# Kernel optimization log

Hardware: AMD Instinct MI355X
Metric: run time of the kernel (lower is better)

## Reference

```python
import jax, jax.numpy as jnp
import numpy as np

EMBED_DIM = 64  # scale factor dim (matches head dim)


def setup_inputs() -> dict:
    key0 = jax.random.key(0)
    kq, kk, kv = jax.random.split(key0, 3)
    shape = (2, 16, 2048, 64)  # [B, H, S, D]
    return {
        "query": jax.random.normal(kq, shape, dtype=jnp.float32),
        "key": jax.random.normal(kk, shape, dtype=jnp.float32),
        "value": jax.random.normal(kv, shape, dtype=jnp.float32),
    }


def reference(query, key, value):
    # qk = Q K^T / sqrt(embed_dim); softmax over last dim; @ V
    inv_scale = jnp.sqrt(jnp.asarray(EMBED_DIM, dtype=query.dtype))
    scores = jnp.einsum("bhqd,bhkd->bhqk", query, key) / inv_scale
    probs = jax.nn.softmax(scores, axis=-1)
    # dropout_p=0.0 -> identity (eval semantics)
    return jnp.einsum("bhqk,bhkd->bhqd", probs, value)
```

## Files before the change

kernel.cpp:

```cpp
#include <hip/hip_runtime.h>
#include <hip/hip_bf16.h>

#define S_LEN 2048
#define DDIM  64
#define NT    (S_LEN / 64)
#define SCALE  0.125f
#define SCALE2 0.18033688f
#define NELEM  4194304
#define NQROW  65536
#define WC_LGKM0 0xc07f

#if __has_builtin(__builtin_amdgcn_permlane32_swap) && __has_builtin(__builtin_amdgcn_permlane16_swap)
#define HAVE_PLSWAP 1
#else
#define HAVE_PLSWAP 0
#endif

typedef __attribute__((ext_vector_type(8))) short short8;
typedef __attribute__((ext_vector_type(4))) float floatx4;

__device__ __forceinline__ short f2bf(float f) {
    union { float f; unsigned u; } v; v.f = f;
    return (short)((v.u + 0x7fffu + ((v.u >> 16) & 1u)) >> 16);
}

__device__ __forceinline__ unsigned pk2bf(float a, float b) {
    union { float f; unsigned u; } x, y; x.f = a; y.f = b;
    unsigned lo = (x.u + 0x7fffu + ((x.u >> 16) & 1u)) >> 16;
    unsigned hi = (y.u + 0x7fffu + ((y.u >> 16) & 1u)) & 0xffff0000u;
    return lo | hi;
}

__device__ __forceinline__ float fexp2(float x) {
#if __has_builtin(__builtin_amdgcn_exp2f)
    return __builtin_amdgcn_exp2f(x);
#else
    return exp2f(x);
#endif
}

#if HAVE_PLSWAP
__device__ __forceinline__ void plswap32(unsigned &a, unsigned &b) {
    auto r = __builtin_amdgcn_permlane32_swap((int)a, (int)b, false, false);
    a = (unsigned)r[0]; b = (unsigned)r[1];
}
__device__ __forceinline__ void plswap16(unsigned &a, unsigned &b) {
    auto r = __builtin_amdgcn_permlane16_swap((int)a, (int)b, false, false);
    a = (unsigned)r[0]; b = (unsigned)r[1];
}
#endif

__global__ __launch_bounds__(256) void prep_kv(const float* __restrict__ K,
                                               const float* __restrict__ V,
                                               short* __restrict__ Kb,
                                               short* __restrict__ Vt) {
    const int bh = blockIdx.x & 31;
    const int st = blockIdx.x >> 5;
    const int t  = threadIdx.x;
    const size_t tile_off = (size_t)bh * (S_LEN * DDIM) + (size_t)st * (64 * DDIM);

    {
        const float* src = K + tile_off + t * 16;
        short* dst = Kb + tile_off + t * 16;
        #pragma unroll
        for (int h = 0; h < 2; ++h) {
            float4 a = *(const float4*)(src + h * 8);
            float4 b = *(const float4*)(src + h * 8 + 4);
            uint4 o;
            o.x = pk2bf(a.x, a.y); o.y = pk2bf(a.z, a.w);
            o.z = pk2bf(b.x, b.y); o.w = pk2bf(b.z, b.w);
            *(uint4*)(dst + h * 8) = o;
        }
    }

    {
        const int s4 = (t & 15) * 4;
        const int d4 = (t >> 4) * 4;
        const float* src = V + tile_off;
        float4 v0 = *(const float4*)(src + (size_t)(s4 + 0) * 64 + d4);
        float4 v1 = *(const float4*)(src + (size_t)(s4 + 1) * 64 + d4);
        float4 v2 = *(const float4*)(src + (size_t)(s4 + 2) * 64 + d4);
        float4 v3 = *(const float4*)(src + (size_t)(s4 + 3) * 64 + d4);
        const float* r0 = (const float*)&v0;
        const float* r1 = (const float*)&v1;
        const float* r2 = (const float*)&v2;
        const float* r3 = (const float*)&v3;
        short* dstb = Vt + (size_t)bh * (DDIM * S_LEN) + (size_t)st * 64 + s4;
        #pragma unroll
        for (int dd = 0; dd < 4; ++dd) {
            uint2 o;
            o.x = pk2bf(r0[dd], r1[dd]);
            o.y = pk2bf(r2[dd], r3[dd]);
            *(uint2*)(dstb + (size_t)(d4 + dd) * S_LEN) = o;
        }
    }
}

__global__ __launch_bounds__(512) void attn_sm8(
    const float* __restrict__ Q, const short* __restrict__ Kb,
    const short* __restrict__ Vt, float* __restrict__ O)
{
    __shared__ short Ks[2][64 * 64];
    __shared__ short Vs[2][64 * 64];
    __shared__ float Dl[128];
#if !HAVE_PLSWAP
    __shared__ short Pl[8][32 * 64];
#endif

    constexpr int NIT = NT / 2;

    const int tid  = threadIdx.x;
    const int wave = tid >> 6;
    const int grp  = wave >> 2;
    const int w4   = wave & 3;
    const int lane = tid & 63;
    const int l16  = lane & 15;
    const int quad = lane >> 4;
    const int x7   = l16 & 7;

    const int bh = blockIdx.x & 31;
    const int qt = blockIdx.x >> 5;
    const int ks = grp;
    const size_t base = (size_t)bh * (S_LEN * DDIM);

    const int g   = tid & 255;
    const int ci0 = g,        r0 = ci0 >> 3, c0 = (ci0 & 7) ^ (r0 & 7);
    const int ci1 = 256 + g,  r1 = ci1 >> 3, c1 = (ci1 & 7) ^ (r1 & 7);
    const size_t koff = (size_t)ks * NIT * (64 * 64);
    const size_t voff = (size_t)ks * NIT * 64;
    const short* pK0 = Kb + base + koff + r0 * 64 + c0 * 8;
    const short* pK1 = Kb + base + koff + r1 * 64 + c1 * 8;
    const short* pV0 = Vt + base + voff + (size_t)r0 * S_LEN + c0 * 8;
    const short* pV1 = Vt + base + voff + (size_t)r1 * S_LEN + c1 * 8;

    short8 rk0 = *(const short8*)pK0;
    short8 rk1 = *(const short8*)pK1;
    short8 rv0 = *(const short8*)pV0;
    short8 rv1 = *(const short8*)pV1;

    short8 qf[2][2];
    #pragma unroll
    for (int nq = 0; nq < 2; ++nq) {
        const float* qp = Q + base + (size_t)(qt * 128 + w4 * 32 + nq * 16 + l16) * 64 + quad * 8;
        #pragma unroll
        for (int kt = 0; kt < 2; ++kt) {
            float4 a = *(const float4*)(qp + kt * 32);
            float4 b = *(const float4*)(qp + kt * 32 + 4);
            union { unsigned u[4]; short8 s; } qc;
            qc.u[0] = pk2bf(a.x * SCALE2, a.y * SCALE2);
            qc.u[1] = pk2bf(a.z * SCALE2, a.w * SCALE2);
            qc.u[2] = pk2bf(b.x * SCALE2, b.y * SCALE2);
            qc.u[3] = pk2bf(b.z * SCALE2, b.w * SCALE2);
            qf[nq][kt] = qc.s;
        }
    }

    floatx4 oacc[2][4];
    float rs[2];
    #pragma unroll
    for (int mt = 0; mt < 2; ++mt) {
        #pragma unroll
        for (int dt = 0; dt < 4; ++dt) oacc[mt][dt] = (floatx4){0.f,0.f,0.f,0.f};
        rs[mt] = 0.f;
    }

    short* Ksg = &Ks[grp][0];
    short* Vsg = &Vs[grp][0];
#if !HAVE_PLSWAP
    short* Pw = &Pl[wave][0];
#endif

    for (int kb = 0; kb < NIT; ++kb) {
        if (kb) __builtin_amdgcn_s_barrier();

        *(short8*)&Ksg[ci0 * 8] = rk0;
        *(short8*)&Ksg[ci1 * 8] = rk1;
        *(short8*)&Vsg[ci0 * 8] = rv0;
        *(short8*)&Vsg[ci1 * 8] = rv1;

        if (kb + 1 < NIT) {
            const int ok = (kb + 1) * (64 * 64), ov = (kb + 1) * 64;
            rk0 = *(const short8*)(pK0 + ok);
            rk1 = *(const short8*)(pK1 + ok);
            rv0 = *(const short8*)(pV0 + ov);
            rv1 = *(const short8*)(pV1 + ov);
        }

        __builtin_amdgcn_s_waitcnt(WC_LGKM0);
        __builtin_amdgcn_s_barrier();

        floatx4 sc[2][4];
        #pragma unroll
        for (int mk = 0; mk < 4; ++mk) {
            floatx4 a0 = (floatx4){0.f,0.f,0.f,0.f};
            floatx4 a1 = (floatx4){0.f,0.f,0.f,0.f};
            #pragma unroll
            for (int kt = 0; kt < 2; ++kt) {
                const int csw = (kt * 4 + quad) ^ x7;
                short8 kf = *(const short8*)&Ksg[(mk * 16 + l16) * 64 + csw * 8];
                a0 = __builtin_amdgcn_mfma_f32_16x16x32_bf16(kf, qf[0][kt], a0, 0, 0, 0);
                a1 = __builtin_amdgcn_mfma_f32_16x16x32_bf16(kf, qf[1][kt], a1, 0, 0, 0);
            }
            sc[0][mk] = a0; sc[1][mk] = a1;
        }

#if HAVE_PLSWAP
        unsigned pa[2][4], pb[2][4];
        #pragma unroll
        for (int nq = 0; nq < 2; ++nq) {
            #pragma unroll
            for (int mk = 0; mk < 4; ++mk) {
                float p0 = fexp2(sc[nq][mk][0]);
                float p1 = fexp2(sc[nq][mk][1]);
                float p2 = fexp2(sc[nq][mk][2]);
                float p3 = fexp2(sc[nq][mk][3]);
                rs[nq] += (p0 + p1) + (p2 + p3);
                pa[nq][mk] = pk2bf(p0, p1);
                pb[nq][mk] = pk2bf(p2, p3);
            }
        }

        #pragma unroll
        for (int kt = 0; kt < 2; ++kt) {
            short8 pf[2];
            #pragma unroll
            for (int nq = 0; nq < 2; ++nq) {
                unsigned a0 = pa[nq][2 * kt], a1 = pa[nq][2 * kt + 1];
                unsigned b0 = pb[nq][2 * kt], b1 = pb[nq][2 * kt + 1];
                plswap32(a0, a1); plswap16(a0, a1);
                plswap32(b0, b1); plswap16(b0, b1);
                union { unsigned u[4]; short8 s; } c;
                c.u[0] = a0; c.u[1] = b0; c.u[2] = a1; c.u[3] = b1;
                pf[nq] = c.s;
            }
            const int csw = (kt * 4 + quad) ^ x7;
            #pragma unroll
            for (int dt = 0; dt < 4; ++dt) {
                short8 vf = *(const short8*)&Vsg[(dt * 16 + l16) * 64 + csw * 8];
                oacc[0][dt] = __builtin_amdgcn_mfma_f32_16x16x32_bf16(pf[0], vf, oacc[0][dt], 0, 0, 0);
                oacc[1][dt] = __builtin_amdgcn_mfma_f32_16x16x32_bf16(pf[1], vf, oacc[1][dt], 0, 0, 0);
            }
        }
#else
        #pragma unroll
        for (int nq = 0; nq < 2; ++nq) {
            const int prow = (nq * 16 + l16) * 64;
            #pragma unroll
            for (int mk = 0; mk < 4; ++mk) {
                float p0 = fexp2(sc[nq][mk][0]);
                float p1 = fexp2(sc[nq][mk][1]);
                float p2 = fexp2(sc[nq][mk][2]);
                float p3 = fexp2(sc[nq][mk][3]);
                rs[nq] += (p0 + p1) + (p2 + p3);
                uint2 pv; pv.x = pk2bf(p0, p1); pv.y = pk2bf(p2, p3);
                const int c8 = (mk * 4 + quad) ^ (2 * x7);
                *(uint2*)&Pw[prow + c8 * 4] = pv;
            }
        }
        #pragma unroll
        for (int kt = 0; kt < 2; ++kt) {
            const int csw = (kt * 4 + quad) ^ x7;
            short8 pf0 = *(const short8*)&Pw[(l16)      * 64 + csw * 8];
            short8 pf1 = *(const short8*)&Pw[(16 + l16) * 64 + csw * 8];
            #pragma unroll
            for (int dt = 0; dt < 4; ++dt) {
                short8 vf = *(const short8*)&Vsg[(dt * 16 + l16) * 64 + csw * 8];
                oacc[0][dt] = __builtin_amdgcn_mfma_f32_16x16x32_bf16(pf0, vf, oacc[0][dt], 0, 0, 0);
                oacc[1][dt] = __builtin_amdgcn_mfma_f32_16x16x32_bf16(pf1, vf, oacc[1][dt], 0, 0, 0);
            }
        }
#endif
    }

    float sred[2];
    #pragma unroll
    for (int nq = 0; nq < 2; ++nq) {
        float s = rs[nq];
        s += __shfl_xor(s, 16, 64);
        s += __shfl_xor(s, 32, 64);
        sred[nq] = s;
    }

    if (grp == 1 && quad == 0) {
        Dl[w4 * 32 + l16]      = sred[0];
        Dl[w4 * 32 + 16 + l16] = sred[1];
    }
    __syncthreads();

    float invt[2];
    if (grp == 0) {
        invt[0] = 1.0f / (sred[0] + Dl[w4 * 32 + l16]);
        invt[1] = 1.0f / (sred[1] + Dl[w4 * 32 + 16 + l16]);
    }

    float* Nb = (float*)&Ks[0][0];
    #pragma unroll
    for (int mt = 0; mt < 2; ++mt) {
        if (grp == 1) {
            #pragma unroll
            for (int dt = 0; dt < 4; ++dt)
                #pragma unroll
                for (int r = 0; r < 4; ++r)
                    Nb[(dt * 4 + r) * 256 + w4 * 64 + lane] = oacc[mt][dt][r];
        }
        __syncthreads();
        if (grp == 0) {
            #pragma unroll
            for (int r = 0; r < 4; ++r) {
                const int row = qt * 128 + w4 * 32 + mt * 16 + quad * 4 + r;
                const float it = __shfl(invt[mt], quad * 4 + r, 64);
                float* op = O + base + (size_t)row * 64 + l16;
                #pragma unroll
                for (int dt = 0; dt < 4; ++dt)
                    op[dt * 16] = (oacc[mt][dt][r] + Nb[(dt * 4 + r) * 256 + w4 * 64 + lane]) * it;
            }
        }
        __syncthreads();
    }
}

#define BQ    64
#define BKEY  64
#define KPAD  72

__global__ __launch_bounds__(256) void attn_kernel(
    const float* __restrict__ Q, const float* __restrict__ K,
    const float* __restrict__ V, float* __restrict__ O)
{
    __shared__ short Ksh[BKEY * KPAD];
    __shared__ short Vtt[DDIM * KPAD];
    __shared__ short Pls[4][16 * KPAD];

    const int tid  = threadIdx.x;
    const int wave = tid >> 6;
    const int lane = tid & 63;
    const int l16  = lane & 15;
    const int quad = lane >> 4;

    const int bh = blockIdx.x & 31;
    const int qt = blockIdx.x >> 5;
    const size_t base = (size_t)bh * S_LEN * DDIM;

    const int qrow = qt * BQ + wave * 16 + l16;
    short8 qf[2];
    {
        const float* qp = Q + base + (size_t)qrow * DDIM + quad * 8;
        #pragma unroll
        for (int kt = 0; kt < 2; ++kt) {
            float4 a = *(const float4*)(qp + kt * 32);
            float4 b = *(const float4*)(qp + kt * 32 + 4);
            short* d = (short*)&qf[kt];
            d[0]=f2bf(a.x*SCALE); d[1]=f2bf(a.y*SCALE); d[2]=f2bf(a.z*SCALE); d[3]=f2bf(a.w*SCALE);
            d[4]=f2bf(b.x*SCALE); d[5]=f2bf(b.y*SCALE); d[6]=f2bf(b.z*SCALE); d[7]=f2bf(b.w*SCALE);
        }
    }

    float m_i[4], l_i[4];
    floatx4 oacc[4];
    #pragma unroll
    for (int r = 0; r < 4; ++r) { m_i[r] = -3.0e38f; l_i[r] = 0.f; }
    #pragma unroll
    for (int dt = 0; dt < 4; ++dt) oacc[dt] = (floatx4){0.f, 0.f, 0.f, 0.f};

    const int skey = tid >> 2;
    const int scol = (tid & 3) * 4;

    for (int kb = 0; kb < S_LEN / BKEY; ++kb) {
        const float* Kg = K + base + (size_t)kb * BKEY * DDIM + (size_t)skey * DDIM;
        const float* Vg = V + base + (size_t)kb * BKEY * DDIM + (size_t)skey * DDIM;
        #pragma unroll
        for (int i = 0; i < 4; ++i) {
            const int c = scol + i * 16;
            float4 kv = *(const float4*)(Kg + c);
            short* kd = &Ksh[skey * KPAD + c];
            kd[0]=f2bf(kv.x); kd[1]=f2bf(kv.y); kd[2]=f2bf(kv.z); kd[3]=f2bf(kv.w);
            float4 vv = *(const float4*)(Vg + c);
            Vtt[(c+0)*KPAD + skey] = f2bf(vv.x);
            Vtt[(c+1)*KPAD + skey] = f2bf(vv.y);
            Vtt[(c+2)*KPAD + skey] = f2bf(vv.z);
            Vtt[(c+3)*KPAD + skey] = f2bf(vv.w);
        }
        __syncthreads();

        floatx4 sc[4];
        #pragma unroll
        for (int nt = 0; nt < 4; ++nt) {
            floatx4 acc = (floatx4){0.f, 0.f, 0.f, 0.f};
            #pragma unroll
            for (int kt = 0; kt < 2; ++kt) {
                short8 kf = *(const short8*)&Ksh[(nt*16 + l16) * KPAD + kt*32 + quad*8];
                acc = __builtin_amdgcn_mfma_f32_16x16x32_bf16(qf[kt], kf, acc, 0, 0, 0);
            }
            sc[nt] = acc;
        }

        short* Pw = &Pls[wave][0];
        #pragma unroll
        for (int r = 0; r < 4; ++r) {
            float mx = fmaxf(fmaxf(sc[0][r], sc[1][r]), fmaxf(sc[2][r], sc[3][r]));
            #pragma unroll
            for (int off = 1; off < 16; off <<= 1)
                mx = fmaxf(mx, __shfl_xor(mx, off, 64));
            const float mnew  = fmaxf(m_i[r], mx);
            const float alpha = __expf(m_i[r] - mnew);
            m_i[r] = mnew;
            float rsum = 0.f;
            #pragma unroll
            for (int nt = 0; nt < 4; ++nt) {
                float p = __expf(sc[nt][r] - mnew);
                rsum += p;
                Pw[(quad*4 + r) * KPAD + nt*16 + l16] = f2bf(p);
            }
            #pragma unroll
            for (int off = 1; off < 16; off <<= 1)
                rsum += __shfl_xor(rsum, off, 64);
            l_i[r] = l_i[r] * alpha + rsum;
            oacc[0][r] *= alpha; oacc[1][r] *= alpha;
            oacc[2][r] *= alpha; oacc[3][r] *= alpha;
        }

        #pragma unroll
        for (int kt = 0; kt < 2; ++kt) {
            short8 pf = *(const short8*)&Pw[l16 * KPAD + kt*32 + quad*8];
            #pragma unroll
            for (int dt = 0; dt < 4; ++dt) {
                short8 vf = *(const short8*)&Vtt[(dt*16 + l16) * KPAD + kt*32 + quad*8];
                oacc[dt] = __builtin_amdgcn_mfma_f32_16x16x32_bf16(pf, vf, oacc[dt], 0, 0, 0);
            }
        }
        __syncthreads();
    }

    #pragma unroll
    for (int r = 0; r < 4; ++r) {
        const float inv = 1.0f / l_i[r];
        const int row = qt * BQ + wave * 16 + quad * 4 + r;
        float* op = O + base + (size_t)row * DDIM + l16;
        #pragma unroll
        for (int dt = 0; dt < 4; ++dt)
            op[dt * 16] = oacc[dt][r] * inv;
    }
}

extern "C" void kernel_launch(void* const* d_in, const int* in_sizes, int n_in,
                              void* d_out, int out_size, void* d_ws, size_t ws_size,
                              hipStream_t stream) {
    const float* Q = (const float*)d_in[0];
    const float* K = (const float*)d_in[1];
    const float* V = (const float*)d_in[2];
    float* O = (float*)d_out;

    const size_t prep_bytes = (size_t)NELEM * 2 * 2;

    if (ws_size >= prep_bytes) {
        short* Kb  = (short*)d_ws;
        short* Vtp = (short*)d_ws + NELEM;
        prep_kv<<<dim3(1024), dim3(256), 0, stream>>>(K, V, Kb, Vtp);
        attn_sm8<<<dim3(512), dim3(512), 0, stream>>>(Q, Kb, Vtp, O);
    } else {
        attn_kernel<<<dim3(1024), dim3(256), 0, stream>>>(Q, K, V, O);
    }
}
```

Before: 144.2 us.

## Double-buffer K/V shared tiles and raise wave priority around MFMA blocks

Splits each group's K and V shared-memory tiles into two buffers. The next tile is written to the alternate buffer while the current one is consumed, which removes one of the two barriers per iteration and overlaps LDS stores with compute. It also wraps the MFMA sections in s_setprio(1)/s_setprio(0) so waves issuing matrix ops are favoured. The cost is twice the LDS for K/V, which may reduce occupancy, plus a prologue that prefetches two tiles ahead.

```diff
diff --git a/kernel.cpp b/kernel.cpp
--- a/kernel.cpp
+++ b/kernel.cpp
@@ -100,8 +100,8 @@
     const float* __restrict__ Q, const short* __restrict__ Kb,
     const short* __restrict__ Vt, float* __restrict__ O)
 {
-    __shared__ short Ks[2][64 * 64];
-    __shared__ short Vs[2][64 * 64];
+    __shared__ short Ks[2][2][64 * 64];
+    __shared__ short Vs[2][2][64 * 64];
     __shared__ float Dl[128];
 #if !HAVE_PLSWAP
     __shared__ short Pl[8][32 * 64];
@@ -164,32 +164,50 @@
         rs[mt] = 0.f;
     }
 
-    short* Ksg = &Ks[grp][0];
-    short* Vsg = &Vs[grp][0];
+    short* Ksg0 = &Ks[grp][0][0];
+    short* Ksg1 = &Ks[grp][1][0];
+    short* Vsg0 = &Vs[grp][0][0];
+    short* Vsg1 = &Vs[grp][1][0];
 #if !HAVE_PLSWAP
     short* Pw = &Pl[wave][0];
 #endif
 
+    *(short8*)&Ksg0[ci0 * 8] = rk0;
+    *(short8*)&Ksg0[ci1 * 8] = rk1;
+    *(short8*)&Vsg0[ci0 * 8] = rv0;
+    *(short8*)&Vsg0[ci1 * 8] = rv1;
+    {
+        const int ok = 64 * 64, ov = 64;
+        rk0 = *(const short8*)(pK0 + ok);
+        rk1 = *(const short8*)(pK1 + ok);
+        rv0 = *(const short8*)(pV0 + ov);
+        rv1 = *(const short8*)(pV1 + ov);
+    }
+    __builtin_amdgcn_s_waitcnt(WC_LGKM0);
+    __builtin_amdgcn_s_barrier();
+
     for (int kb = 0; kb < NIT; ++kb) {
-        if (kb) __builtin_amdgcn_s_barrier();
-
-        *(short8*)&Ksg[ci0 * 8] = rk0;
-        *(short8*)&Ksg[ci1 * 8] = rk1;
-        *(short8*)&Vsg[ci0 * 8] = rv0;
-        *(short8*)&Vsg[ci1 * 8] = rv1;
+        short* Ksc = (kb & 1) ? Ksg1 : Ksg0;
+        short* Vsc = (kb & 1) ? Vsg1 : Vsg0;
+        short* Ksn = (kb & 1) ? Ksg0 : Ksg1;
+        short* Vsn = (kb & 1) ? Vsg0 : Vsg1;
 
         if (kb + 1 < NIT) {
-            const int ok = (kb + 1) * (64 * 64), ov = (kb + 1) * 64;
-            rk0 = *(const short8*)(pK0 + ok);
-            rk1 = *(const short8*)(pK1 + ok);
-            rv0 = *(const short8*)(pV0 + ov);
-            rv1 = *(const short8*)(pV1 + ov);
-        }
-
-        __builtin_amdgcn_s_waitcnt(WC_LGKM0);
-        __builtin_amdgcn_s_barrier();
+            *(short8*)&Ksn[ci0 * 8] = rk0;
+            *(short8*)&Ksn[ci1 * 8] = rk1;
+            *(short8*)&Vsn[ci0 * 8] = rv0;
+            *(short8*)&Vsn[ci1 * 8] = rv1;
+            if (kb + 2 < NIT) {
+                const int ok = (kb + 2) * (64 * 64), ov = (kb + 2) * 64;
+                rk0 = *(const short8*)(pK0 + ok);
+                rk1 = *(const short8*)(pK1 + ok);
+                rv0 = *(const short8*)(pV0 + ov);
+                rv1 = *(const short8*)(pV1 + ov);
+            }
+        }
 
         floatx4 sc[2][4];
+        __builtin_amdgcn_s_setprio(1);
         #pragma unroll
         for (int mk = 0; mk < 4; ++mk) {
             floatx4 a0 = (floatx4){0.f,0.f,0.f,0.f};
@@ -197,12 +215,13 @@
             #pragma unroll
             for (int kt = 0; kt < 2; ++kt) {
                 const int csw = (kt * 4 + quad) ^ x7;
-                short8 kf = *(const short8*)&Ksg[(mk * 16 + l16) * 64 + csw * 8];
+                short8 kf = *(const short8*)&Ksc[(mk * 16 + l16) * 64 + csw * 8];
                 a0 = __builtin_amdgcn_mfma_f32_16x16x32_bf16(kf, qf[0][kt], a0, 0, 0, 0);
                 a1 = __builtin_amdgcn_mfma_f32_16x16x32_bf16(kf, qf[1][kt], a1, 0, 0, 0);
             }
             sc[0][mk] = a0; sc[1][mk] = a1;
         }
+        __builtin_amdgcn_s_setprio(0);
 
 #if HAVE_PLSWAP
         unsigned pa[2][4], pb[2][4];
@@ -234,12 +253,14 @@
                 pf[nq] = c.s;
             }
             const int csw = (kt * 4 + quad) ^ x7;
+            __builtin_amdgcn_s_setprio(1);
             #pragma unroll
             for (int dt = 0; dt < 4; ++dt) {
-                short8 vf = *(const short8*)&Vsg[(dt * 16 + l16) * 64 + csw * 8];
+                short8 vf = *(const short8*)&Vsc[(dt * 16 + l16) * 64 + csw * 8];
                 oacc[0][dt] = __builtin_amdgcn_mfma_f32_16x16x32_bf16(pf[0], vf, oacc[0][dt], 0, 0, 0);
                 oacc[1][dt] = __builtin_amdgcn_mfma_f32_16x16x32_bf16(pf[1], vf, oacc[1][dt], 0, 0, 0);
             }
+            __builtin_amdgcn_s_setprio(0);
         }
 #else
         #pragma unroll
@@ -264,12 +285,15 @@
             short8 pf1 = *(const short8*)&Pw[(16 + l16) * 64 + csw * 8];
             #pragma unroll
             for (int dt = 0; dt < 4; ++dt) {
-                short8 vf = *(const short8*)&Vsg[(dt * 16 + l16) * 64 + csw * 8];
+                short8 vf = *(const short8*)&Vsc[(dt * 16 + l16) * 64 + csw * 8];
                 oacc[0][dt] = __builtin_amdgcn_mfma_f32_16x16x32_bf16(pf0, vf, oacc[0][dt], 0, 0, 0);
                 oacc[1][dt] = __builtin_amdgcn_mfma_f32_16x16x32_bf16(pf1, vf, oacc[1][dt], 0, 0, 0);
             }
         }
 #endif
+
+        __builtin_amdgcn_s_waitcnt(WC_LGKM0);
+        __builtin_amdgcn_s_barrier();
     }
 
     float sred[2];
@@ -293,7 +317,7 @@
         invt[1] = 1.0f / (sred[1] + Dl[w4 * 32 + 16 + l16]);
     }
 
-    float* Nb = (float*)&Ks[0][0];
+    float* Nb = (float*)&Ks[0][0][0];
     #pragma unroll
     for (int mt = 0; mt < 2; ++mt) {
         if (grp == 1) {
```

Result: no change. 146.3 us (+1.4%).

## Load V fragments directly into registers and split epilogue across both groups

Applied to the files above, without the earlier changes.

Removes V staging through shared memory. Each lane now loads its MFMA V operand fragments straight from global memory into registers, and the next block is prefetched after the PV MFMAs. The epilogue is also rebalanced so that both wave groups exchange partial accumulators through a dedicated shared buffer and each writes half the output rows, which removes the serialized two-pass reduction. The trade-offs are higher register pressure and less coalesced global loads for V, and the permlane swap path is now unconditional.

```diff
diff --git a/kernel.cpp b/kernel.cpp
--- a/kernel.cpp
+++ b/kernel.cpp
@@ -10,12 +10,6 @@
 #define NQROW  65536
 #define WC_LGKM0 0xc07f
 
-#if __has_builtin(__builtin_amdgcn_permlane32_swap) && __has_builtin(__builtin_amdgcn_permlane16_swap)
-#define HAVE_PLSWAP 1
-#else
-#define HAVE_PLSWAP 0
-#endif
-
 typedef __attribute__((ext_vector_type(8))) short short8;
 typedef __attribute__((ext_vector_type(4))) float floatx4;
 
@@ -39,7 +33,6 @@
 #endif
 }
 
-#if HAVE_PLSWAP
 __device__ __forceinline__ void plswap32(unsigned &a, unsigned &b) {
     auto r = __builtin_amdgcn_permlane32_swap((int)a, (int)b, false, false);
     a = (unsigned)r[0]; b = (unsigned)r[1];
@@ -48,7 +41,6 @@
     auto r = __builtin_amdgcn_permlane16_swap((int)a, (int)b, false, false);
     a = (unsigned)r[0]; b = (unsigned)r[1];
 }
-#endif
 
 __global__ __launch_bounds__(256) void prep_kv(const float* __restrict__ K,
                                                const float* __restrict__ V,
@@ -98,14 +90,12 @@
 
 __global__ __launch_bounds__(512) void attn_sm8(
     const float* __restrict__ Q, const short* __restrict__ Kb,
-    const short* __restrict__ Vt, float* __restrict__ O)
+    const float* __restrict__ Vt_unused, float* __restrict__ O,
+    const short* __restrict__ Vt)
 {
     __shared__ short Ks[2][64 * 64];
-    __shared__ short Vs[2][64 * 64];
+    __shared__ float Nbuf[2][4096];
     __shared__ float Dl[128];
-#if !HAVE_PLSWAP
-    __shared__ short Pl[8][32 * 64];
-#endif
 
     constexpr int NIT = NT / 2;
 
@@ -130,13 +120,16 @@
     const size_t voff = (size_t)ks * NIT * 64;
     const short* pK0 = Kb + base + koff + r0 * 64 + c0 * 8;
     const short* pK1 = Kb + base + koff + r1 * 64 + c1 * 8;
-    const short* pV0 = Vt + base + voff + (size_t)r0 * S_LEN + c0 * 8;
-    const short* pV1 = Vt + base + voff + (size_t)r1 * S_LEN + c1 * 8;
+    const short* pVf = Vt + base + voff + (size_t)l16 * S_LEN + quad * 8;
 
     short8 rk0 = *(const short8*)pK0;
     short8 rk1 = *(const short8*)pK1;
-    short8 rv0 = *(const short8*)pV0;
-    short8 rv1 = *(const short8*)pV1;
+    short8 vreg[2][4];
+    #pragma unroll
+    for (int kt = 0; kt < 2; ++kt)
+        #pragma unroll
+        for (int dt = 0; dt < 4; ++dt)
+            vreg[kt][dt] = *(const short8*)(pVf + (size_t)dt * 16 * S_LEN + kt * 32);
 
     short8 qf[2][2];
     #pragma unroll
@@ -160,30 +153,22 @@
     #pragma unroll
     for (int mt = 0; mt < 2; ++mt) {
         #pragma unroll
-        for (int dt = 0; dt < 4; ++dt) oacc[mt][dt] = (floatx4){0.f,0.f,0.f,0.f};
+        for (int dt = 0; dt < 4; ++dt) oacc[mt][dt] = (floatx4){0.f, 0.f, 0.f, 0.f};
         rs[mt] = 0.f;
     }
 
     short* Ksg = &Ks[grp][0];
-    short* Vsg = &Vs[grp][0];
-#if !HAVE_PLSWAP
-    short* Pw = &Pl[wave][0];
-#endif
 
     for (int kb = 0; kb < NIT; ++kb) {
         if (kb) __builtin_amdgcn_s_barrier();
 
         *(short8*)&Ksg[ci0 * 8] = rk0;
         *(short8*)&Ksg[ci1 * 8] = rk1;
-        *(short8*)&Vsg[ci0 * 8] = rv0;
-        *(short8*)&Vsg[ci1 * 8] = rv1;
 
         if (kb + 1 < NIT) {
-            const int ok = (kb + 1) * (64 * 64), ov = (kb + 1) * 64;
+            const int ok = (kb + 1) * (64 * 64);
             rk0 = *(const short8*)(pK0 + ok);
             rk1 = *(const short8*)(pK1 + ok);
-            rv0 = *(const short8*)(pV0 + ov);
-            rv1 = *(const short8*)(pV1 + ov);
         }
 
         __builtin_amdgcn_s_waitcnt(WC_LGKM0);
@@ -192,8 +177,8 @@
         floatx4 sc[2][4];
         #pragma unroll
         for (int mk = 0; mk < 4; ++mk) {
-            floatx4 a0 = (floatx4){0.f,0.f,0.f,0.f};
-            floatx4 a1 = (floatx4){0.f,0.f,0.f,0.f};
+            floatx4 a0 = (floatx4){0.f, 0.f, 0.f, 0.f};
+            floatx4 a1 = (floatx4){0.f, 0.f, 0.f, 0.f};
             #pragma unroll
             for (int kt = 0; kt < 2; ++kt) {
                 const int csw = (kt * 4 + quad) ^ x7;
@@ -204,7 +189,6 @@
             sc[0][mk] = a0; sc[1][mk] = a1;
         }
 
-#if HAVE_PLSWAP
         unsigned pa[2][4], pb[2][4];
         #pragma unroll
         for (int nq = 0; nq < 2; ++nq) {
@@ -233,43 +217,21 @@
                 c.u[0] = a0; c.u[1] = b0; c.u[2] = a1; c.u[3] = b1;
                 pf[nq] = c.s;
             }
-            const int csw = (kt * 4 + quad) ^ x7;
             #pragma unroll
             for (int dt = 0; dt < 4; ++dt) {
-                short8 vf = *(const short8*)&Vsg[(dt * 16 + l16) * 64 + csw * 8];
-                oacc[0][dt] = __builtin_amdgcn_mfma_f32_16x16x32_bf16(pf[0], vf, oacc[0][dt], 0, 0, 0);
-                oacc[1][dt] = __builtin_amdgcn_mfma_f32_16x16x32_bf16(pf[1], vf, oacc[1][dt], 0, 0, 0);
-            }
-        }
-#else
-        #pragma unroll
-        for (int nq = 0; nq < 2; ++nq) {
-            const int prow = (nq * 16 + l16) * 64;
-            #pragma unroll
-            for (int mk = 0; mk < 4; ++mk) {
-                float p0 = fexp2(sc[nq][mk][0]);
-                float p1 = fexp2(sc[nq][mk][1]);
-                float p2 = fexp2(sc[nq][mk][2]);
-                float p3 = fexp2(sc[nq][mk][3]);
-                rs[nq] += (p0 + p1) + (p2 + p3);
-                uint2 pv; pv.x = pk2bf(p0, p1); pv.y = pk2bf(p2, p3);
-                const int c8 = (mk * 4 + quad) ^ (2 * x7);
-                *(uint2*)&Pw[prow + c8 * 4] = pv;
-            }
-        }
-        #pragma unroll
-        for (int kt = 0; kt < 2; ++kt) {
-            const int csw = (kt * 4 + quad) ^ x7;
-            short8 pf0 = *(const short8*)&Pw[(l16)      * 64 + csw * 8];
-            short8 pf1 = *(const short8*)&Pw[(16 + l16) * 64 + csw * 8];
-            #pragma unroll
-            for (int dt = 0; dt < 4; ++dt) {
-                short8 vf = *(const short8*)&Vsg[(dt * 16 + l16) * 64 + csw * 8];
-                oacc[0][dt] = __builtin_amdgcn_mfma_f32_16x16x32_bf16(pf0, vf, oacc[0][dt], 0, 0, 0);
-                oacc[1][dt] = __builtin_amdgcn_mfma_f32_16x16x32_bf16(pf1, vf, oacc[1][dt], 0, 0, 0);
-            }
-        }
-#endif
+                oacc[0][dt] = __builtin_amdgcn_mfma_f32_16x16x32_bf16(pf[0], vreg[kt][dt], oacc[0][dt], 0, 0, 0);
+                oacc[1][dt] = __builtin_amdgcn_mfma_f32_16x16x32_bf16(pf[1], vreg[kt][dt], oacc[1][dt], 0, 0, 0);
+            }
+        }
+
+        if (kb + 1 < NIT) {
+            const int ov = (kb + 1) * 64;
+            #pragma unroll
+            for (int kt = 0; kt < 2; ++kt)
+                #pragma unroll
+                for (int dt = 0; dt < 4; ++dt)
+                    vreg[kt][dt] = *(const short8*)(pVf + (size_t)dt * 16 * S_LEN + ov + kt * 32);
+        }
     }
 
     float sred[2];
@@ -281,41 +243,36 @@
         sred[nq] = s;
     }
 
-    if (grp == 1 && quad == 0) {
-        Dl[w4 * 32 + l16]      = sred[0];
-        Dl[w4 * 32 + 16 + l16] = sred[1];
+    if (quad == 0) {
+        if (grp == 1) Dl[w4 * 32 + l16]      = sred[0];
+        else          Dl[w4 * 32 + 16 + l16] = sred[1];
+    }
+
+    {
+        float* NbMine = &Nbuf[grp][0];
+        const int pmt = 1 - grp;
+        #pragma unroll
+        for (int dt = 0; dt < 4; ++dt)
+            #pragma unroll
+            for (int r = 0; r < 4; ++r)
+                NbMine[(dt * 4 + r) * 256 + w4 * 64 + lane] = oacc[pmt][dt][r];
     }
     __syncthreads();
 
-    float invt[2];
-    if (grp == 0) {
-        invt[0] = 1.0f / (sred[0] + Dl[w4 * 32 + l16]);
-        invt[1] = 1.0f / (sred[1] + Dl[w4 * 32 + 16 + l16]);
-    }
-
-    float* Nb = (float*)&Ks[0][0];
-    #pragma unroll
-    for (int mt = 0; mt < 2; ++mt) {
-        if (grp == 1) {
+    {
+        const float* NbOther = &Nbuf[1 - grp][0];
+        const int cmt = grp;
+        const float dother = Dl[w4 * 32 + (grp ? 16 : 0) + l16];
+        const float invc = 1.0f / (sred[cmt] + dother);
+        #pragma unroll
+        for (int r = 0; r < 4; ++r) {
+            const int row = qt * 128 + w4 * 32 + cmt * 16 + quad * 4 + r;
+            const float it = __shfl(invc, quad * 4 + r, 64);
+            float* op = O + base + (size_t)row * 64 + l16;
             #pragma unroll
             for (int dt = 0; dt < 4; ++dt)
-                #pragma unroll
-                for (int r = 0; r < 4; ++r)
-                    Nb[(dt * 4 + r) * 256 + w4 * 64 + lane] = oacc[mt][dt][r];
-        }
-        __syncthreads();
-        if (grp == 0) {
-            #pragma unroll
-            for (int r = 0; r < 4; ++r) {
-                const int row = qt * 128 + w4 * 32 + mt * 16 + quad * 4 + r;
-                const float it = __shfl(invt[mt], quad * 4 + r, 64);
-                float* op = O + base + (size_t)row * 64 + l16;
-                #pragma unroll
-                for (int dt = 0; dt < 4; ++dt)
-                    op[dt * 16] = (oacc[mt][dt][r] + Nb[(dt * 4 + r) * 256 + w4 * 64 + lane]) * it;
-            }
-        }
-        __syncthreads();
+                op[dt * 16] = (oacc[cmt][dt][r] + NbOther[(dt * 4 + r) * 256 + w4 * 64 + lane]) * it;
+        }
     }
 }
 
@@ -456,7 +413,7 @@
         short* Kb  = (short*)d_ws;
         short* Vtp = (short*)d_ws + NELEM;
         prep_kv<<<dim3(1024), dim3(256), 0, stream>>>(K, V, Kb, Vtp);
-        attn_sm8<<<dim3(512), dim3(512), 0, stream>>>(Q, Kb, Vtp, O);
+        attn_sm8<<<dim3(512), dim3(512), 0, stream>>>(Q, Kb, nullptr, O, Vtp);
     } else {
         attn_kernel<<<dim3(1024), dim3(256), 0, stream>>>(Q, K, V, O);
     }
```

New measurement: 185.6 us. 28.7% more time.
